# Optimization experiments

Hardware: AMD Instinct MI355X
Metric: run time of the kernel (lower is better)

## Reference

```python
import jax, jax.numpy as jnp
import numpy as np

D_MODEL = 1024
N_HEADS = 16
D_K = D_MODEL // N_HEADS
BATCH = 8
SEQ = 1024
ROPE_BASE = 10000.0


def setup_inputs() -> dict:
    key = jax.random.key(0)
    ks = jax.random.split(key, 9)
    s = 1.0 / np.sqrt(D_MODEL)
    return {
        "x": jax.random.normal(ks[0], (BATCH, SEQ, D_MODEL), dtype=jnp.float32),
        "position_ids": jnp.arange(SEQ, dtype=jnp.int32)[None, :],
        "Wq": jax.random.normal(ks[1], (D_MODEL, D_MODEL), dtype=jnp.float32) * s,
        "bq": jnp.zeros((D_MODEL,), dtype=jnp.float32),
        "Wk": jax.random.normal(ks[2], (D_MODEL, D_MODEL), dtype=jnp.float32) * s,
        "bk": jnp.zeros((D_MODEL,), dtype=jnp.float32),
        "Wv": jax.random.normal(ks[3], (D_MODEL, D_MODEL), dtype=jnp.float32) * s,
        "bv": jnp.zeros((D_MODEL,), dtype=jnp.float32),
        "Wo": jax.random.normal(ks[4], (D_MODEL, D_MODEL), dtype=jnp.float32) * s,
        "bo": jnp.zeros((D_MODEL,), dtype=jnp.float32),
    }


def _apply_rope(t, position_ids):
    # t: [B, H, S, D_K]; position_ids: [1, S] (broadcast over batch)
    half = D_K // 2
    inv_freq = 1.0 / (ROPE_BASE ** (jnp.arange(half, dtype=jnp.float32) * 2.0 / D_K))
    ang = position_ids.astype(jnp.float32)[..., None] * inv_freq  # [1, S, half]
    cos = jnp.cos(ang)[:, None, :, :]  # [1, 1, S, half]
    sin = jnp.sin(ang)[:, None, :, :]
    t1, t2 = jnp.split(t, 2, axis=-1)
    return jnp.concatenate([t1 * cos - t2 * sin, t1 * sin + t2 * cos], axis=-1)


def reference(x, position_ids, Wq, bq, Wk, bk, Wv, bv, Wo, bo):
    B, S, D = x.shape
    def proj(W, b):
        # torch Linear: x @ W.T + b
        y = jnp.einsum('bsd,ed->bse', x, W) + b
        return y.reshape(B, S, N_HEADS, D_K).transpose(0, 2, 1, 3)  # [B,H,S,Dk]
    Q = proj(Wq, bq)
    K = proj(Wk, bk)
    V = proj(Wv, bv)
    Q = _apply_rope(Q, position_ids)
    K = _apply_rope(K, position_ids)
    scores = jnp.einsum('bhqd,bhkd->bhqk', Q, K) / jnp.sqrt(jnp.float32(D_K))
    attn = jax.nn.softmax(scores, axis=-1)
    out = jnp.einsum('bhqk,bhkd->bhqd', attn, V)
    out = out.transpose(0, 2, 1, 3).reshape(B, S, D)
    return jnp.einsum('bsd,ed->bse', out, Wo) + bo
```

## Files before the change

### kernel.cpp

```cpp
#include <hip/hip_runtime.h>
#include <hip/hip_bf16.h>


typedef __bf16 bf16_t;
typedef __bf16 bf16x8 __attribute__((ext_vector_type(8)));
typedef float  f32x4  __attribute__((ext_vector_type(4)));

static __device__ __forceinline__ f32x4 mfma16(bf16x8 a, bf16x8 b, f32x4 c) {
  return __builtin_amdgcn_mfma_f32_16x16x32_bf16(a, b, c, 0, 0, 0);
}

#if __has_builtin(__builtin_amdgcn_exp2f)
#define EXP2F(x) __builtin_amdgcn_exp2f(x)
#else
#define EXP2F(x) exp2f(x)
#endif

__global__ void k_prep(const float* __restrict__ x, const float* __restrict__ Wq,
                       const float* __restrict__ Wk, const float* __restrict__ Wv,
                       const float* __restrict__ Wo, const int* __restrict__ pos,
                       bf16_t* __restrict__ Xf, bf16_t* __restrict__ Wf,
                       float2* __restrict__ rt) {
  const int bid = blockIdx.x;
  const int t = threadIdx.x;
  if (bid < 4096) {
    int g = bid * 256 + t;
    int rg = g >> 11, kt = (g >> 6) & 31, lane = g & 63;
    int m = rg * 16 + (lane & 15);
    int k = kt * 32 + (lane >> 4) * 8;
    const float* s = x + (size_t)m * 1024 + k;
    float4 v0 = *(const float4*)s;
    float4 v1 = *(const float4*)(s + 4);
    union { bf16_t b[8]; } pk;
    pk.b[0] = (bf16_t)v0.x; pk.b[1] = (bf16_t)v0.y; pk.b[2] = (bf16_t)v0.z; pk.b[3] = (bf16_t)v0.w;
    pk.b[4] = (bf16_t)v1.x; pk.b[5] = (bf16_t)v1.y; pk.b[6] = (bf16_t)v1.z; pk.b[7] = (bf16_t)v1.w;
    __builtin_memcpy(Xf + (size_t)g * 8, pk.b, 16);
  } else if (bid < 6144) {
    int g = (bid - 4096) * 256 + t;
    int rg = g >> 11, kt = (g >> 6) & 31, lane = g & 63;
    const float* src = (rg < 64) ? Wq : (rg < 128) ? Wk : (rg < 192) ? Wv : Wo;
    int row = (rg & 63) * 16 + (lane & 15);
    int k = kt * 32 + (lane >> 4) * 8;
    const float* s = src + (size_t)row * 1024 + k;
    float4 v0 = *(const float4*)s;
    float4 v1 = *(const float4*)(s + 4);
    union { bf16_t b[8]; } pk;
    pk.b[0] = (bf16_t)v0.x; pk.b[1] = (bf16_t)v0.y; pk.b[2] = (bf16_t)v0.z; pk.b[3] = (bf16_t)v0.w;
    pk.b[4] = (bf16_t)v1.x; pk.b[5] = (bf16_t)v1.y; pk.b[6] = (bf16_t)v1.z; pk.b[7] = (bf16_t)v1.w;
    __builtin_memcpy(Wf + (size_t)g * 8, pk.b, 16);
  } else {
    int rb = bid - 6144;
    int s = rb * 8 + (t >> 5);
    int f = t & 31;
    float p = (float)pos[s];
    float inv = powf(10000.0f, -(float)(2 * f) / 64.0f);
    float a = p * inv;
    rt[s * 32 + f] = make_float2(cosf(a), sinf(a));
  }
}

#define GEMM_WIDE_BODY(AfBase, BfBase)                                         \
  const int t = threadIdx.x;                                                   \
  const int lane = t & 63, w = t >> 6;                         \
  const int hi = lane >> 4, c = lane & 15;                                     \
  const int wm = w >> 1, wn = w & 1;                                           \
  const bf16_t* Ab = (AfBase) + (size_t)((i0 >> 4) + wm * 8) * 16384 + lane * 8; \
  const bf16_t* Bb = (BfBase) + (size_t)((e0 >> 4) + wn * 4) * 16384 + lane * 8; \
  bf16x8 pA[8], pB[4], qA[8], qB[4];                                           \
  f32x4 acc[8][4] = {};                                                        \
  auto loadP = [&](int kt) {                                                   \
    _Pragma("unroll") for (int f = 0; f < 8; ++f)                              \
      pA[f] = *(const bf16x8*)(Ab + (size_t)f * 16384 + kt * 512);             \
    _Pragma("unroll") for (int f = 0; f < 4; ++f)                              \
      pB[f] = *(const bf16x8*)(Bb + (size_t)f * 16384 + kt * 512);             \
  };                                                                           \
  auto loadQ = [&](int kt) {                                                   \
    _Pragma("unroll") for (int f = 0; f < 8; ++f)                              \
      qA[f] = *(const bf16x8*)(Ab + (size_t)f * 16384 + kt * 512);             \
    _Pragma("unroll") for (int f = 0; f < 4; ++f)                              \
      qB[f] = *(const bf16x8*)(Bb + (size_t)f * 16384 + kt * 512);             \
  };                                                                           \
  auto compP = [&]() {                                                         \
    __builtin_amdgcn_s_setprio(1);                                             \
    _Pragma("unroll") for (int fr = 0; fr < 8; ++fr)                           \
      _Pragma("unroll") for (int nc = 0; nc < 4; ++nc)                         \
        acc[fr][nc] = mfma16(pA[fr], pB[nc], acc[fr][nc]);                     \
    __builtin_amdgcn_s_setprio(0);                                             \
  };                                                                           \
  auto compQ = [&]() {                                                         \
    __builtin_amdgcn_s_setprio(1);                                             \
    _Pragma("unroll") for (int fr = 0; fr < 8; ++fr)                           \
      _Pragma("unroll") for (int nc = 0; nc < 4; ++nc)                         \
        acc[fr][nc] = mfma16(qA[fr], qB[nc], acc[fr][nc]);                     \
    __builtin_amdgcn_s_setprio(0);                                             \
  };                                                                           \
  loadP(0);                                                                    \
  loadQ(1);                                                                    \
  _Pragma("unroll 3")                                                          \
  for (int jj = 0; jj < 15; ++jj) {                                            \
    compP(); loadP(jj * 2 + 2);                                                \
    compQ(); loadQ(jj * 2 + 3);                                                \
  }                                                                            \
  compP();                                                                     \
  compQ();

__global__ __launch_bounds__(256) void k_gemm_qkv(
    const bf16_t* __restrict__ Xf, const bf16_t* __restrict__ Wf,
    const float* __restrict__ bq, const float* __restrict__ bk,
    const float* __restrict__ bv, const float2* __restrict__ rt,
    bf16_t* __restrict__ Qh, bf16_t* __restrict__ Kg, bf16_t* __restrict__ Vg) {
  const int bid = blockIdx.x;
  const int x = bid & 7, q = bid >> 3;
  const int i0 = (x * 4 + (q & 3)) * 256;
  const int e0 = (q >> 2) * 128;

  GEMM_WIDE_BODY(Xf, Wf)

  const int z = e0 >> 10;
  const int ez0 = (e0 & 1023) + wn * 64;
  const int h = ez0 >> 6;
  const float* bias = (z == 0) ? bq : (z == 1) ? bk : bv;
  if (z == 2) {
#pragma unroll
    for (int fr = 0; fr < 8; ++fr) {
      int i = i0 + wm * 128 + fr * 16 + hi * 4;
      int b_ = i >> 10, sbase = i & 1023;
      int bhv = b_ * 16 + h;
      int lane_ = c | (((sbase >> 3) & 3) << 4);
#pragma unroll
      for (int nc = 0; nc < 4; ++nc) {
        float bv_ = bias[ez0 + nc * 16 + c];
        union { bf16_t b[4]; } pk;
#pragma unroll
        for (int r = 0; r < 4; ++r) pk.b[r] = (bf16_t)(acc[fr][nc][r] + bv_);
        size_t g = (size_t)(bhv * 4 + nc) * 32 + (sbase >> 5);
        __builtin_memcpy(&Vg[g * 512 + lane_ * 8 + (sbase & 7)], pk.b, 8);
      }
    }
  } else if (z == 0) {
    const float scl = 0.18033688011112042f;
#pragma unroll
    for (int fr = 0; fr < 8; ++fr) {
      int i = i0 + wm * 128 + fr * 16 + hi * 4;
      int b_ = i >> 10, sbase = i & 1023;
      size_t obase = (size_t)((b_ * 16 + h) * 1024);
#pragma unroll
      for (int nc = 0; nc < 2; ++nc) {
        int f = nc * 16 + c;
        float b1_ = bias[ez0 + f], b2_ = bias[ez0 + f + 32];
#pragma unroll
        for (int r = 0; r < 4; ++r) {
          int s = sbase + r;
          float2 cs = rt[s * 32 + f];
          float q1 = acc[fr][nc][r] + b1_;
          float q2 = acc[fr][nc + 2][r] + b2_;
          Qh[(obase + s) * 64 + f] = (bf16_t)((q1 * cs.x - q2 * cs.y) * scl);
          Qh[(obase + s) * 64 + f + 32] = (bf16_t)((q1 * cs.y + q2 * cs.x) * scl);
        }
      }
    }
  } else {
#pragma unroll
    for (int fr = 0; fr < 8; ++fr) {
      int i = i0 + wm * 128 + fr * 16 + hi * 4;
      int b_ = i >> 10, sbase = i & 1023;
      bf16_t* gb = Kg + (size_t)((b_ * 16 + h) * 64 + (sbase >> 4)) * 1024;
#pragma unroll
      for (int nc = 0; nc < 2; ++nc) {
        int f = nc * 16 + c;
        float b1_ = bias[ez0 + f], b2_ = bias[ez0 + f + 32];
        int laneHi = (nc * 2 + (c >> 3)) << 4;
#pragma unroll
        for (int r = 0; r < 4; ++r) {
          int s = sbase + r;
          float2 cs = rt[s * 32 + f];
          float q1 = acc[fr][nc][r] + b1_;
          float q2 = acc[fr][nc + 2][r] + b2_;
          size_t off = (size_t)((hi * 4 + r) | laneHi) * 8 + (c & 7);
          gb[off] = (bf16_t)(q1 * cs.x - q2 * cs.y);
          gb[off + 512] = (bf16_t)(q1 * cs.y + q2 * cs.x);
        }
      }
    }
  }
}

__global__ __launch_bounds__(256) void k_gemm_out(
    const bf16_t* __restrict__ Ogf, const bf16_t* __restrict__ Wf,
    const float* __restrict__ bo, float* __restrict__ out) {
  const int bid = blockIdx.x;
  const int x = bid & 7, q = bid >> 3;
  const int i0 = (x * 4 + (q & 3)) * 256;
  const int e0 = (q >> 2) * 128;
  const bf16_t* WfO = Wf + (size_t)192 * 16384;

  GEMM_WIDE_BODY(Ogf, WfO)

#pragma unroll
  for (int fr = 0; fr < 8; ++fr) {
    int i = i0 + wm * 128 + fr * 16 + hi * 4;
#pragma unroll
    for (int nc = 0; nc < 4; ++nc) {
      int e = e0 + wn * 64 + nc * 16 + c;
      float bv_ = bo[e];
#pragma unroll
      for (int r = 0; r < 4; ++r)
        out[(size_t)(i + r) * 1024 + e] = acc[fr][nc][r] + bv_;
    }
  }
}

__global__ __launch_bounds__(512) void k_attn(
    const bf16_t* __restrict__ Qh, const bf16_t* __restrict__ Kg,
    const bf16_t* __restrict__ Vg, bf16_t* __restrict__ Ogf) {
  __shared__ alignas(16) char PL[8][2048];
  const int t = threadIdx.x;
  const int lane = t & 63, w = t >> 6;
  const int hi = lane >> 4, c = lane & 15;
  const int bid = blockIdx.x;
  const int wg = (bid & 7) * 32 + (bid >> 3);
  const int bh = wg >> 1, half = wg & 1;
  const int q0 = half * 512 + w * 64;
  const size_t qbase = (size_t)bh * 64 * 1024;

  const bf16_t* Kb = Kg + (size_t)bh * 65536 + lane * 8;
  const bf16_t* Vb = Vg + (size_t)bh * 65536 + lane * 8;

  bf16x8 qf[4][2];
#pragma unroll
  for (int ss = 0; ss < 4; ++ss)
#pragma unroll
    for (int kk = 0; kk < 2; ++kk)
      qf[ss][kk] = *(const bf16x8*)&Qh[qbase + (size_t)(q0 + ss * 16 + c) * 64 +
                                       kk * 32 + hi * 8];

  f32x4 o[4][4] = {};
  float m_[4] = {-1e30f, -1e30f, -1e30f, -1e30f};
  float l_[4] = {0.f, 0.f, 0.f, 0.f};
  char* const plw = &PL[w][0];

  bf16x8 kp[8], kq[8], vv[8];
#pragma unroll
  for (int i = 0; i < 8; ++i) kp[i] = *(const bf16x8*)(Kb + i * 512);

#define SM_PV(ST, M, L, O)                                                     \
  {                                                                            \
    float pmax = -1e30f;                                                       \
    _Pragma("unroll") for (int ni = 0; ni < 4; ++ni)                           \
      _Pragma("unroll") for (int r = 0; r < 4; ++r)                            \
        pmax = fmaxf(pmax, ST[ni][r]);                                         \
    pmax = fmaxf(pmax, __shfl_xor(pmax, 16));                                  \
    pmax = fmaxf(pmax, __shfl_xor(pmax, 32));                                  \
    if (!__all(pmax <= M + 8.0f)) {                 \
      float mn = fmaxf(M, pmax);                                               \
      float sc = EXP2F(M - mn);                                                \
      M = mn;                                                                  \
      L *= sc;                                                                 \
      _Pragma("unroll") for (int od = 0; od < 4; ++od)                         \
        _Pragma("unroll") for (int r = 0; r < 4; ++r) O[od][r] *= sc;          \
    }                                                                          \
    float psum = 0.f;                                                          \
    _Pragma("unroll") for (int ni = 0; ni < 4; ++ni) {                         \
      union { bf16_t b[4]; } pk;                                               \
      _Pragma("unroll") for (int r = 0; r < 4; ++r) {                          \
        float p = EXP2F(ST[ni][r] - M);                                        \
        psum += p;                                                             \
        pk.b[r] = (bf16_t)p;                                                   \
      }                                                                        \
      __builtin_memcpy(plw + (ni * 2 + (hi >> 1)) * 256 + c * 16 + (hi & 1) * 8, \
                       pk.b, 8);                                               \
    }                                                                          \
    psum += __shfl_xor(psum, 16);                                              \
    psum += __shfl_xor(psum, 32);                                              \
    L += psum;                                                                 \
    bf16x8 pa[2];                                                              \
    __builtin_memcpy(&pa[0], plw + lane * 16, 16);                             \
    __builtin_memcpy(&pa[1], plw + 1024 + lane * 16, 16);                      \
    _Pragma("unroll") for (int od = 0; od < 4; ++od)                           \
      _Pragma("unroll") for (int kk = 0; kk < 2; ++kk)                         \
        O[od] = mfma16(vv[od * 2 + kk], pa[kk], O[od]);                        \
  }

#define ATTN_TILE(KS, KN, KT)                                                  \
  {                                                                            \
    _Pragma("unroll") for (int i = 0; i < 8; ++i)                              \
      vv[i] = *(const bf16x8*)(Vb + ((i >> 1) * 32 + (KT) * 2 + (i & 1)) * 512); \
    _Pragma("unroll") for (int ss = 0; ss < 4; ++ss) {                         \
      f32x4 st[4] = {};                                                        \
      _Pragma("unroll") for (int ni = 0; ni < 4; ++ni)                         \
        _Pragma("unroll") for (int kk = 0; kk < 2; ++kk)                       \
          st[ni] = mfma16(KS[ni * 2 + kk], qf[ss][kk], st[ni]);                \
      if (ss == 0 && (KT) + 1 < 16) {                                          \
        _Pragma("unroll") for (int i = 0; i < 8; ++i)                          \
          KN[i] = *(const bf16x8*)(Kb + (((KT) + 1) * 8 + i) * 512);           \
      }                                                                        \
      SM_PV(st, m_[ss], l_[ss], o[ss])                                         \
    }                                                                          \
  }

  for (int jj = 0; jj < 8; ++jj) {
    ATTN_TILE(kp, kq, jj * 2);
    ATTN_TILE(kq, kp, jj * 2 + 1);
  }
#undef ATTN_TILE
#undef SM_PV

  int b_ = bh >> 4, h = bh & 15;
  int rg0 = ((b_ << 10) + q0) >> 4;
#pragma unroll
  for (int ss = 0; ss < 4; ++ss) {
    float iv = 1.f / l_[ss];
#pragma unroll
    for (int od = 0; od < 4; ++od) {
      union { bf16_t b[4]; } pk;
#pragma unroll
      for (int r = 0; r < 4; ++r) pk.b[r] = (bf16_t)(o[ss][od][r] * iv);
      int kt2 = (h << 1) + (od >> 1);
      int lp = ((od & 1) * 2 + (hi >> 1)) * 16 + c;
      int el = (hi & 1) * 4;
      __builtin_memcpy(&Ogf[((size_t)((rg0 + ss) * 32 + kt2) * 64 + lp) * 8 + el],
                       pk.b, 8);
    }
  }
}

extern "C" void kernel_launch(void* const* d_in, const int* in_sizes, int n_in,
                              void* d_out, int out_size, void* d_ws, size_t ws_size,
                              hipStream_t stream) {
  const float* x = (const float*)d_in[0];
  const int* pos = (const int*)d_in[1];
  const float* Wq = (const float*)d_in[2];
  const float* bq = (const float*)d_in[3];
  const float* Wk = (const float*)d_in[4];
  const float* bk = (const float*)d_in[5];
  const float* Wv = (const float*)d_in[6];
  const float* bv = (const float*)d_in[7];
  const float* Wo = (const float*)d_in[8];
  const float* bo = (const float*)d_in[9];
  float* out = (float*)d_out;

  char* ws = (char*)d_ws;
  bf16_t* Xf = (bf16_t*)ws;
  bf16_t* Wf = (bf16_t*)(ws + (16u << 20));
  bf16_t* Vg = (bf16_t*)(ws + (24u << 20));
  float2* rt = (float2*)(ws + (42u << 20));
  bf16_t* Qh = (bf16_t*)d_out;
  bf16_t* Kg = (bf16_t*)d_out + (size_t)8 * 1024 * 1024;
  bf16_t* Ogf = Xf;

  k_prep<<<6272, 256, 0, stream>>>(x, Wq, Wk, Wv, Wo, pos, Xf, Wf, rt);
  k_gemm_qkv<<<768, 256, 0, stream>>>(Xf, Wf, bq, bk, bv, rt, Qh, Kg, Vg);
  k_attn<<<256, 512, 0, stream>>>(Qh, Kg, Vg, Ogf);
  k_gemm_out<<<256, 256, 0, stream>>>(Ogf, Wf, bo, out);
}
```

Before: 133.7 us.

## Switch projection GEMMs to 32x32x16 MFMA with matching fragment layout

Both projection GEMMs (QKV and output) now use the 32x32x16 bf16 MFMA instead of 16x16x32. The prep kernel's pre-swizzled X and W layouts, the GEMM fragment loads, all epilogues (RoPE, K/V scatter, output store) and the attention output write are rewritten to the 32-row fragment layout. The larger MFMA shape cuts the number of operand fragment loads per output tile and may raise matrix-core throughput. The cost is a new index mapping everywhere, which risks layout bugs, and strided epilogue stores.

```diff
diff --git a/kernel.cpp b/kernel.cpp
--- a/kernel.cpp
+++ b/kernel.cpp
@@ -5,9 +5,13 @@
 typedef __bf16 bf16_t;
 typedef __bf16 bf16x8 __attribute__((ext_vector_type(8)));
 typedef float  f32x4  __attribute__((ext_vector_type(4)));
+typedef float  f32x16 __attribute__((ext_vector_type(16)));
 
 static __device__ __forceinline__ f32x4 mfma16(bf16x8 a, bf16x8 b, f32x4 c) {
   return __builtin_amdgcn_mfma_f32_16x16x32_bf16(a, b, c, 0, 0, 0);
+}
+static __device__ __forceinline__ f32x16 mfma32(bf16x8 a, bf16x8 b, f32x16 c) {
+  return __builtin_amdgcn_mfma_f32_32x32x16_bf16(a, b, c, 0, 0, 0);
 }
 
 #if __has_builtin(__builtin_amdgcn_exp2f)
@@ -25,9 +29,9 @@
   const int t = threadIdx.x;
   if (bid < 4096) {
     int g = bid * 256 + t;
-    int rg = g >> 11, kt = (g >> 6) & 31, lane = g & 63;
-    int m = rg * 16 + (lane & 15);
-    int k = kt * 32 + (lane >> 4) * 8;
+    int rg = g >> 12, kt = (g >> 6) & 63, lane = g & 63;
+    int m = rg * 32 + (lane & 31);
+    int k = kt * 16 + (lane >> 5) * 8;
     const float* s = x + (size_t)m * 1024 + k;
     float4 v0 = *(const float4*)s;
     float4 v1 = *(const float4*)(s + 4);
@@ -37,10 +41,10 @@
     __builtin_memcpy(Xf + (size_t)g * 8, pk.b, 16);
   } else if (bid < 6144) {
     int g = (bid - 4096) * 256 + t;
-    int rg = g >> 11, kt = (g >> 6) & 31, lane = g & 63;
-    const float* src = (rg < 64) ? Wq : (rg < 128) ? Wk : (rg < 192) ? Wv : Wo;
-    int row = (rg & 63) * 16 + (lane & 15);
-    int k = kt * 32 + (lane >> 4) * 8;
+    int rg = g >> 12, kt = (g >> 6) & 63, lane = g & 63;
+    const float* src = (rg < 32) ? Wq : (rg < 64) ? Wk : (rg < 96) ? Wv : Wo;
+    int row = (rg & 31) * 32 + (lane & 31);
+    int k = kt * 16 + (lane >> 5) * 8;
     const float* s = src + (size_t)row * 1024 + k;
     float4 v0 = *(const float4*)s;
     float4 v1 = *(const float4*)(s + 4);
@@ -62,42 +66,42 @@
 #define GEMM_WIDE_BODY(AfBase, BfBase)                                         \
   const int t = threadIdx.x;                                                   \
   const int lane = t & 63, w = t >> 6;                         \
-  const int hi = lane >> 4, c = lane & 15;                                     \
+  const int c5 = lane & 31, h2 = lane >> 5;                                    \
   const int wm = w >> 1, wn = w & 1;                                           \
-  const bf16_t* Ab = (AfBase) + (size_t)((i0 >> 4) + wm * 8) * 16384 + lane * 8; \
-  const bf16_t* Bb = (BfBase) + (size_t)((e0 >> 4) + wn * 4) * 16384 + lane * 8; \
-  bf16x8 pA[8], pB[4], qA[8], qB[4];                                           \
-  f32x4 acc[8][4] = {};                                                        \
+  const bf16_t* Ab = (AfBase) + (size_t)((i0 >> 5) + wm * 4) * 32768 + lane * 8; \
+  const bf16_t* Bb = (BfBase) + (size_t)((e0 >> 5) + wn * 2) * 32768 + lane * 8; \
+  bf16x8 pA[4], pB[2], qA[4], qB[2];                                           \
+  f32x16 acc[4][2] = {};                                                       \
   auto loadP = [&](int kt) {                                                   \
-    _Pragma("unroll") for (int f = 0; f < 8; ++f)                              \
-      pA[f] = *(const bf16x8*)(Ab + (size_t)f * 16384 + kt * 512);             \
     _Pragma("unroll") for (int f = 0; f < 4; ++f)                              \
-      pB[f] = *(const bf16x8*)(Bb + (size_t)f * 16384 + kt * 512);             \
+      pA[f] = *(const bf16x8*)(Ab + (size_t)f * 32768 + kt * 512);             \
+    _Pragma("unroll") for (int f = 0; f < 2; ++f)                              \
+      pB[f] = *(const bf16x8*)(Bb + (size_t)f * 32768 + kt * 512);             \
   };                                                                           \
   auto loadQ = [&](int kt) {                                                   \
-    _Pragma("unroll") for (int f = 0; f < 8; ++f)                              \
-      qA[f] = *(const bf16x8*)(Ab + (size_t)f * 16384 + kt * 512);             \
     _Pragma("unroll") for (int f = 0; f < 4; ++f)                              \
-      qB[f] = *(const bf16x8*)(Bb + (size_t)f * 16384 + kt * 512);             \
+      qA[f] = *(const bf16x8*)(Ab + (size_t)f * 32768 + kt * 512);             \
+    _Pragma("unroll") for (int f = 0; f < 2; ++f)                              \
+      qB[f] = *(const bf16x8*)(Bb + (size_t)f * 32768 + kt * 512);             \
   };                                                                           \
   auto compP = [&]() {                                                         \
     __builtin_amdgcn_s_setprio(1);                                             \
-    _Pragma("unroll") for (int fr = 0; fr < 8; ++fr)                           \
-      _Pragma("unroll") for (int nc = 0; nc < 4; ++nc)                         \
-        acc[fr][nc] = mfma16(pA[fr], pB[nc], acc[fr][nc]);                     \
+    _Pragma("unroll") for (int fr = 0; fr < 4; ++fr)                           \
+      _Pragma("unroll") for (int nc = 0; nc < 2; ++nc)                         \
+        acc[fr][nc] = mfma32(pA[fr], pB[nc], acc[fr][nc]);                     \
     __builtin_amdgcn_s_setprio(0);                                             \
   };                                                                           \
   auto compQ = [&]() {                                                         \
     __builtin_amdgcn_s_setprio(1);                                             \
-    _Pragma("unroll") for (int fr = 0; fr < 8; ++fr)                           \
-      _Pragma("unroll") for (int nc = 0; nc < 4; ++nc)                         \
-        acc[fr][nc] = mfma16(qA[fr], qB[nc], acc[fr][nc]);                     \
+    _Pragma("unroll") for (int fr = 0; fr < 4; ++fr)                           \
+      _Pragma("unroll") for (int nc = 0; nc < 2; ++nc)                         \
+        acc[fr][nc] = mfma32(qA[fr], qB[nc], acc[fr][nc]);                     \
     __builtin_amdgcn_s_setprio(0);                                             \
   };                                                                           \
   loadP(0);                                                                    \
   loadQ(1);                                                                    \
   _Pragma("unroll 3")                                                          \
-  for (int jj = 0; jj < 15; ++jj) {                                            \
+  for (int jj = 0; jj < 31; ++jj) {                                            \
     compP(); loadP(jj * 2 + 2);                                                \
     compQ(); loadQ(jj * 2 + 3);                                                \
   }                                                                            \
@@ -120,68 +124,64 @@
   const int ez0 = (e0 & 1023) + wn * 64;
   const int h = ez0 >> 6;
   const float* bias = (z == 0) ? bq : (z == 1) ? bk : bv;
+  const int i0w = i0 + wm * 128;
+  const int b_ = i0w >> 10, sl0 = i0w & 1023;
+
   if (z == 2) {
-#pragma unroll
-    for (int fr = 0; fr < 8; ++fr) {
-      int i = i0 + wm * 128 + fr * 16 + hi * 4;
-      int b_ = i >> 10, sbase = i & 1023;
-      int bhv = b_ * 16 + h;
-      int lane_ = c | (((sbase >> 3) & 3) << 4);
-#pragma unroll
-      for (int nc = 0; nc < 4; ++nc) {
-        float bv_ = bias[ez0 + nc * 16 + c];
-        union { bf16_t b[4]; } pk;
-#pragma unroll
-        for (int r = 0; r < 4; ++r) pk.b[r] = (bf16_t)(acc[fr][nc][r] + bv_);
-        size_t g = (size_t)(bhv * 4 + nc) * 32 + (sbase >> 5);
-        __builtin_memcpy(&Vg[g * 512 + lane_ * 8 + (sbase & 7)], pk.b, 8);
+    const int bhv = b_ * 16 + h;
+#pragma unroll
+    for (int fr = 0; fr < 4; ++fr) {
+#pragma unroll
+      for (int nc = 0; nc < 2; ++nc) {
+        float bv_ = bias[ez0 + nc * 32 + c5];
+        size_t gbase = ((size_t)(bhv * 4 + nc * 2 + (c5 >> 4)) * 32 +
+                        (sl0 >> 5) + fr) * 512;
+#pragma unroll
+        for (int q_ = 0; q_ < 4; ++q_) {
+          union { bf16_t b[4]; } pk;
+#pragma unroll
+          for (int r = 0; r < 4; ++r) pk.b[r] = (bf16_t)(acc[fr][nc][4 * q_ + r] + bv_);
+          __builtin_memcpy(&Vg[gbase + (size_t)((c5 & 15) | (q_ << 4)) * 8 + h2 * 4],
+                           pk.b, 8);
+        }
       }
     }
   } else if (z == 0) {
     const float scl = 0.18033688011112042f;
-#pragma unroll
-    for (int fr = 0; fr < 8; ++fr) {
-      int i = i0 + wm * 128 + fr * 16 + hi * 4;
-      int b_ = i >> 10, sbase = i & 1023;
-      size_t obase = (size_t)((b_ * 16 + h) * 1024);
-#pragma unroll
-      for (int nc = 0; nc < 2; ++nc) {
-        int f = nc * 16 + c;
-        float b1_ = bias[ez0 + f], b2_ = bias[ez0 + f + 32];
+    const float b1_ = bias[ez0 + c5], b2_ = bias[ez0 + 32 + c5];
+    size_t obase = (size_t)((b_ * 16 + h)) * 1024;
+#pragma unroll
+    for (int fr = 0; fr < 4; ++fr)
+#pragma unroll
+      for (int q_ = 0; q_ < 4; ++q_)
 #pragma unroll
         for (int r = 0; r < 4; ++r) {
-          int s = sbase + r;
-          float2 cs = rt[s * 32 + f];
-          float q1 = acc[fr][nc][r] + b1_;
-          float q2 = acc[fr][nc + 2][r] + b2_;
-          Qh[(obase + s) * 64 + f] = (bf16_t)((q1 * cs.x - q2 * cs.y) * scl);
-          Qh[(obase + s) * 64 + f + 32] = (bf16_t)((q1 * cs.y + q2 * cs.x) * scl);
+          int sl = sl0 + fr * 32 + 8 * q_ + 4 * h2 + r;
+          float2 cs = rt[sl * 32 + c5];
+          float q1 = acc[fr][0][4 * q_ + r] + b1_;
+          float q2 = acc[fr][1][4 * q_ + r] + b2_;
+          Qh[(obase + sl) * 64 + c5] = (bf16_t)((q1 * cs.x - q2 * cs.y) * scl);
+          Qh[(obase + sl) * 64 + c5 + 32] = (bf16_t)((q1 * cs.y + q2 * cs.x) * scl);
         }
-      }
-    }
   } else {
-#pragma unroll
-    for (int fr = 0; fr < 8; ++fr) {
-      int i = i0 + wm * 128 + fr * 16 + hi * 4;
-      int b_ = i >> 10, sbase = i & 1023;
-      bf16_t* gb = Kg + (size_t)((b_ * 16 + h) * 64 + (sbase >> 4)) * 1024;
-#pragma unroll
-      for (int nc = 0; nc < 2; ++nc) {
-        int f = nc * 16 + c;
-        float b1_ = bias[ez0 + f], b2_ = bias[ez0 + f + 32];
-        int laneHi = (nc * 2 + (c >> 3)) << 4;
+    const float b1_ = bias[ez0 + c5], b2_ = bias[ez0 + 32 + c5];
+    bf16_t* gb0 = Kg + (size_t)((b_ * 16 + h) * 64) * 1024;
+    const int lane16hi = ((c5 >> 3) & 3) << 4;
+#pragma unroll
+    for (int fr = 0; fr < 4; ++fr)
+#pragma unroll
+      for (int q_ = 0; q_ < 4; ++q_)
 #pragma unroll
         for (int r = 0; r < 4; ++r) {
-          int s = sbase + r;
-          float2 cs = rt[s * 32 + f];
-          float q1 = acc[fr][nc][r] + b1_;
-          float q2 = acc[fr][nc + 2][r] + b2_;
-          size_t off = (size_t)((hi * 4 + r) | laneHi) * 8 + (c & 7);
-          gb[off] = (bf16_t)(q1 * cs.x - q2 * cs.y);
-          gb[off + 512] = (bf16_t)(q1 * cs.y + q2 * cs.x);
+          int sl = sl0 + fr * 32 + 8 * q_ + 4 * h2 + r;
+          float2 cs = rt[sl * 32 + c5];
+          float q1 = acc[fr][0][4 * q_ + r] + b1_;
+          float q2 = acc[fr][1][4 * q_ + r] + b2_;
+          bf16_t* gbs = gb0 + (size_t)(sl >> 4) * 1024;
+          size_t off = (size_t)((sl & 15) | lane16hi) * 8 + (c5 & 7);
+          gbs[off] = (bf16_t)(q1 * cs.x - q2 * cs.y);
+          gbs[off + 512] = (bf16_t)(q1 * cs.y + q2 * cs.x);
         }
-      }
-    }
   }
 }
 
@@ -192,22 +192,25 @@
   const int x = bid & 7, q = bid >> 3;
   const int i0 = (x * 4 + (q & 3)) * 256;
   const int e0 = (q >> 2) * 128;
-  const bf16_t* WfO = Wf + (size_t)192 * 16384;
+  const bf16_t* WfO = Wf + (size_t)96 * 32768;
 
   GEMM_WIDE_BODY(Ogf, WfO)
 
-#pragma unroll
-  for (int fr = 0; fr < 8; ++fr) {
-    int i = i0 + wm * 128 + fr * 16 + hi * 4;
-#pragma unroll
-    for (int nc = 0; nc < 4; ++nc) {
-      int e = e0 + wn * 64 + nc * 16 + c;
+  const int i0w = i0 + wm * 128;
+#pragma unroll
+  for (int fr = 0; fr < 4; ++fr)
+#pragma unroll
+    for (int nc = 0; nc < 2; ++nc) {
+      int e = e0 + wn * 64 + nc * 32 + c5;
       float bv_ = bo[e];
 #pragma unroll
-      for (int r = 0; r < 4; ++r)
-        out[(size_t)(i + r) * 1024 + e] = acc[fr][nc][r] + bv_;
+      for (int q_ = 0; q_ < 4; ++q_)
+#pragma unroll
+        for (int r = 0; r < 4; ++r) {
+          int i = i0w + fr * 32 + 8 * q_ + 4 * h2 + r;
+          out[(size_t)i * 1024 + e] = acc[fr][nc][4 * q_ + r] + bv_;
+        }
     }
-  }
 }
 
 __global__ __launch_bounds__(512) void k_attn(
@@ -306,19 +309,19 @@
 #undef SM_PV
 
   int b_ = bh >> 4, h = bh & 15;
-  int rg0 = ((b_ << 10) + q0) >> 4;
+  int rgb = ((b_ << 10) + q0) >> 5;
 #pragma unroll
   for (int ss = 0; ss < 4; ++ss) {
     float iv = 1.f / l_[ss];
+    int rg32 = rgb + (ss >> 1);
+    int l32 = ((ss & 1) * 16 + c) | ((hi >> 1) << 5);
 #pragma unroll
     for (int od = 0; od < 4; ++od) {
       union { bf16_t b[4]; } pk;
 #pragma unroll
       for (int r = 0; r < 4; ++r) pk.b[r] = (bf16_t)(o[ss][od][r] * iv);
-      int kt2 = (h << 1) + (od >> 1);
-      int lp = ((od & 1) * 2 + (hi >> 1)) * 16 + c;
-      int el = (hi & 1) * 4;
-      __builtin_memcpy(&Ogf[((size_t)((rg0 + ss) * 32 + kt2) * 64 + lp) * 8 + el],
+      int kt16 = h * 4 + od;
+      __builtin_memcpy(&Ogf[((size_t)(rg32 * 64 + kt16) * 64 + l32) * 8 + (hi & 1) * 4],
                        pk.b, 8);
     }
   }
```

Result: slower. 136.6 us (+2.2%).
